# Performance work log

Hardware: AMD Instinct MI355X
Metric: run time of the kernel (lower is better)

Reference implementation:

```python
import jax, jax.numpy as jnp
import numpy as np

B, T, C = 16, 2048, 384
HEAD = 384

def setup_inputs() -> dict:
    key = jax.random.key(0)
    kx, kq, kk, kv = jax.random.split(key, 4)
    s = 1.0 / np.sqrt(C)
    return {
        "x": jax.random.normal(kx, (B, T, C), dtype=jnp.float32),
        "Wq": jax.random.normal(kq, (C, HEAD), dtype=jnp.float32) * s,
        "Wk": jax.random.normal(kk, (C, HEAD), dtype=jnp.float32) * s,
        "Wv": jax.random.normal(kv, (C, HEAD), dtype=jnp.float32) * s,
    }

def reference(x, Wq, Wk, Wv):
    # x: [B,T,C]; single causal attention head, eval mode (dropout = identity)
    Bc, Tc, Cc = x.shape
    q = jnp.einsum('btc,ch->bth', x, Wq)
    k = jnp.einsum('btc,ch->bth', x, Wk)
    v = jnp.einsum('btc,ch->bth', x, Wv)
    # NOTE: original scales by C**-0.5 (embedding dim), not head_size**-0.5
    scale = Cc ** (-0.5)
    wei = jnp.einsum('bth,bsh->bts', q, k) * scale  # [B,T,T]
    causal = jnp.tril(jnp.ones((Tc, Tc), dtype=bool))
    wei = jnp.where(causal, wei, -jnp.inf)
    wei = jax.nn.softmax(wei, axis=-1)
    out = jnp.einsum('bts,bsh->bth', wei, v)  # [B,T,head]
    return out
```

## Files before the change

kernel.cpp:

```cpp
#include <hip/hip_runtime.h>
#include <hip/hip_bf16.h>

#define NB 16
#define TT 2048
#define CC 384

typedef short bf16x8 __attribute__((ext_vector_type(8)));
typedef float f32x4 __attribute__((ext_vector_type(4)));

static __device__ __forceinline__ short f2bf(float f) {
  union { __hip_bfloat16 h; short s; } u;
  u.h = __float2bfloat16(f);
  return u.s;
}

#define QSC (0.051031036307982884f * 1.4426950408889634f)

__global__ __launch_bounds__(384)
void conv_wt(const float* __restrict__ Wq, const float* __restrict__ Wk,
             const float* __restrict__ Wv, short* __restrict__ Wbt) {
  const int w = blockIdx.x / CC;
  const int n = blockIdx.x % CC;
  const int k = threadIdx.x;
  const float* W = (w == 0) ? Wq : (w == 1) ? Wk : Wv;
  Wbt[((size_t)w * CC + n) * CC + k] = f2bf(W[(size_t)k * CC + n]);
}

__global__ __launch_bounds__(256)
void xconv(const float* __restrict__ x, short* __restrict__ xb) {
  const int i = (blockIdx.x * 256 + threadIdx.x) * 8;
  const float4 a = *(const float4*)(x + i);
  const float4 c = *(const float4*)(x + i + 4);
  bf16x8 r;
  r[0] = f2bf(a.x); r[1] = f2bf(a.y); r[2] = f2bf(a.z); r[3] = f2bf(a.w);
  r[4] = f2bf(c.x); r[5] = f2bf(c.y); r[6] = f2bf(c.z); r[7] = f2bf(c.w);
  *(bf16x8*)(xb + i) = r;
}

__global__ __launch_bounds__(256, 3)
void proj_gemm(const short* __restrict__ xb, const short* __restrict__ Wbt,
               short* __restrict__ Q, short* __restrict__ K,
               short* __restrict__ Vt) {
  __shared__ char smem[34816];
  short* Es = (short*)smem;

  const int mt = blockIdx.x & 255;
  const int nt = blockIdx.x >> 8;
  const int wsel = nt / 3;
  const int nc0 = (nt % 3) * 128;
  const int tid = threadIdx.x;
  const int wave = tid >> 6, lane = tid & 63;
  const int l15 = lane & 15, quad = lane >> 4;
  const int wm = (wave & 1) * 64, wn = (wave >> 1) * 64;

  const short* Ab = xb + (size_t)mt * 128 * CC;
  const short* Bb = Wbt + ((size_t)wsel * CC + nc0) * CC;

  int aoff[2];
  #pragma unroll
  for (int j = 0; j < 2; ++j) {
    const int lin = wave * 2048 + j * 1024 + lane * 16;
    const int r = lin >> 6;
    const int s = (lin >> 4) & 3;
    aoff[j] = r * CC + ((s ^ ((r >> 1) & 3)) * 8);
  }
  char* AW = smem + wave * 2048;
  char* BW = smem + 16384 + wave * 2048;

  f32x4 acc[16];
  #pragma unroll
  for (int i = 0; i < 16; ++i) acc[i] = f32x4{0.f, 0.f, 0.f, 0.f};

  #pragma unroll
  for (int pc = 0; pc < 2; ++pc) {
    #pragma unroll
    for (int j = 0; j < 2; ++j)
      __builtin_amdgcn_global_load_lds(
          (const __attribute__((address_space(1))) void*)(Ab + pc * 32 + aoff[j]),
          (__attribute__((address_space(3))) void*)(AW + pc * 8192 + j * 1024), 16, 0, 0);
    #pragma unroll
    for (int j = 0; j < 2; ++j)
      __builtin_amdgcn_global_load_lds(
          (const __attribute__((address_space(1))) void*)(Bb + pc * 32 + aoff[j]),
          (__attribute__((address_space(3))) void*)(BW + pc * 8192 + j * 1024), 16, 0, 0);
  }

  for (int kt = 0; kt < 12; ++kt) {
    const int kb = kt & 1;
    if (kt == 11) {
      asm volatile("s_waitcnt vmcnt(0)" ::: "memory");
    } else {
      asm volatile("s_waitcnt vmcnt(4)" ::: "memory");
    }
    __builtin_amdgcn_s_barrier();
    __builtin_amdgcn_sched_barrier(0);

    const char* As = smem + kb * 8192;
    const char* Bs = smem + 16384 + kb * 8192;
    bf16x8 af[4], bf[4];
    #pragma unroll
    for (int i = 0; i < 4; ++i) {
      const int ar = wm + i * 16 + l15;
      const int br = wn + i * 16 + l15;
      af[i] = *(const bf16x8*)(As + ar * 64 + ((quad ^ ((ar >> 1) & 3)) << 4));
      bf[i] = *(const bf16x8*)(Bs + br * 64 + ((quad ^ ((br >> 1) & 3)) << 4));
    }
    #pragma unroll
    for (int i = 0; i < 4; ++i)
      #pragma unroll
      for (int j = 0; j < 4; ++j)
        acc[i * 4 + j] =
            __builtin_amdgcn_mfma_f32_16x16x32_bf16(af[i], bf[j], acc[i * 4 + j], 0, 0, 0);

    __builtin_amdgcn_sched_barrier(0);
    __builtin_amdgcn_s_barrier();
    if (kt + 2 < 12) {
      const int k0 = (kt + 2) * 32;
      #pragma unroll
      for (int j = 0; j < 2; ++j)
        __builtin_amdgcn_global_load_lds(
            (const __attribute__((address_space(1))) void*)(Ab + k0 + aoff[j]),
            (__attribute__((address_space(3))) void*)(AW + kb * 8192 + j * 1024), 16, 0, 0);
      #pragma unroll
      for (int j = 0; j < 2; ++j)
        __builtin_amdgcn_global_load_lds(
            (const __attribute__((address_space(1))) void*)(Bb + k0 + aoff[j]),
            (__attribute__((address_space(3))) void*)(BW + kb * 8192 + j * 1024), 16, 0, 0);
    }
  }

  if (nt < 6) {
    short* O = (nt < 3) ? Q : K;
    const float sc = (nt < 3) ? QSC : 1.0f;
    #pragma unroll
    for (int i = 0; i < 4; ++i)
      #pragma unroll
      for (int j = 0; j < 4; ++j) {
        const f32x4 a = acc[i * 4 + j];
        const int r0 = mt * 128 + wm + i * 16 + quad * 4;
        const int c = nc0 + wn + j * 16 + l15;
        #pragma unroll
        for (int r = 0; r < 4; ++r) O[(size_t)(r0 + r) * CC + c] = f2bf(a[r] * sc);
      }
  } else {
    __syncthreads();
    #pragma unroll
    for (int i = 0; i < 4; ++i)
      #pragma unroll
      for (int j = 0; j < 4; ++j) {
        const f32x4 a = acc[i * 4 + j];
        const int dl = wn + j * 16 + l15;
        const int ml = wm + i * 16 + quad * 4;
        short4 p4;
        p4.x = f2bf(a[0]); p4.y = f2bf(a[1]); p4.z = f2bf(a[2]); p4.w = f2bf(a[3]);
        *(short4*)(Es + (size_t)dl * 136 + ml) = p4;
      }
    __syncthreads();
    const int d0 = (nt - 6) * 128;
    const int b = mt >> 4, t0 = (mt & 15) * 128;
    const int dr = tid >> 1, hf = tid & 1;
    const short* src = Es + (size_t)dr * 136 + hf * 64;
    short* dst = Vt + ((size_t)b * CC + d0 + dr) * TT + t0 + hf * 64;
    #pragma unroll
    for (int c = 0; c < 8; ++c)
      *(bf16x8*)(dst + c * 8) = *(const bf16x8*)(src + c * 8);
  }
}


#define ATTN_PRELUDE                                                          \
  __shared__ char sm[54272];                                                  \
  char* KsS = sm;                                                             \
  char* VsS = sm + 24576;                                                     \
  const int tid = threadIdx.x;                                                \
  const int wave = tid >> 6, lane = tid & 63;                                 \
  const int l15 = lane & 15, quad = lane >> 4;                                \
  short* pw = (short*)(sm + 49152) + wave * 640;                              \
  bf16x8 onesf;                                                               \
  _Pragma("unroll")                                                           \
  for (int i = 0; i < 8; ++i) onesf[i] = (short)0x3F80;                       \
  int koff[6], voff[6];                                                       \
  _Pragma("unroll")                                                           \
  for (int j = 0; j < 6; ++j) {                                               \
    const int lin = wave * 6144 + j * 1024 + lane * 16;                       \
    const int kr = lin / 768;                                                 \
    const int ksl = (lin - kr * 768) >> 4;                                    \
    koff[j] = kr * 768 + ((ksl ^ (kr & 7)) << 4);                             \
    const int vr = lin >> 6;                                                  \
    const int vsl = (lin >> 4) & 3;                                           \
    voff[j] = vr * 4096 + (((vsl - (vr >> 2)) & 3) << 4);                     \
  }                                                                           \
  char* KsW = KsS + wave * 6144;                                              \
  char* VsW = VsS + wave * 6144;

#define STAGE_CHUNK(ck)                                                       \
  do {                                                                        \
    const size_t kby_ = (size_t)(ck) * 24576;                                 \
    const size_t vby_ = (size_t)(ck) * 64;                                    \
    _Pragma("unroll")                                                         \
    for (int j = 0; j < 6; ++j)                                               \
      __builtin_amdgcn_global_load_lds(                                       \
          (const __attribute__((address_space(1))) void*)(kbB + kby_ + koff[j]), \
          (__attribute__((address_space(3))) void*)(KsW + j * 1024), 16, 0, 0);  \
    _Pragma("unroll")                                                         \
    for (int j = 0; j < 6; ++j)                                               \
      __builtin_amdgcn_global_load_lds(                                       \
          (const __attribute__((address_space(1))) void*)(vtB + vby_ + voff[j]), \
          (__attribute__((address_space(3))) void*)(VsW + j * 1024), 16, 0, 0);  \
  } while (0)

#define CHUNK_LOOP(C0, C1)                                                    \
  for (int kc = (C0); kc < (C1); ++kc) {                                      \
    const int k0 = kc * 32;                                                   \
    const int kb = (kc - (C0)) & 1;                                           \
    if (kc + 1 == (C1)) {                                                     \
      asm volatile("s_waitcnt vmcnt(0)" ::: "memory");                        \
    } else {                                                                  \
      asm volatile("s_waitcnt vmcnt(12)" ::: "memory");                       \
    }                                                                         \
    __builtin_amdgcn_s_barrier();                                             \
    __builtin_amdgcn_sched_barrier(0);                                        \
    const bool active = (k0 <= q0 + 15);                                      \
    if (active) {                                                             \
      const char* Ksb = KsS + kb * 0;             \
      (void)Ksb;                                                              \
    }                                                                         \
  }


__global__ __launch_bounds__(256, 2)
void attn_plain(const short* __restrict__ Q, const short* __restrict__ K,
                const short* __restrict__ Vt, float* __restrict__ out) {
  ATTN_PRELUDE
  const int blk = blockIdx.x;
  const int qt = 31 - (blk >> 4);
  const int b  = blk & 15;
  const int q0 = qt * 64 + wave * 16;

  bf16x8 qf[12];
  const short* qp = Q + ((size_t)b * TT + q0 + l15) * CC + quad * 8;
  #pragma unroll
  for (int ks = 0; ks < 12; ++ks) qf[ks] = *(const bf16x8*)(qp + ks * 32);

  f32x4 o[24];
  #pragma unroll
  for (int n = 0; n < 24; ++n) o[n] = f32x4{0.f, 0.f, 0.f, 0.f};
  f32x4 lsum = f32x4{0.f, 0.f, 0.f, 0.f};
  float m[4];
  #pragma unroll
  for (int r = 0; r < 4; ++r) m[r] = -INFINITY;

  const char* kbB = (const char*)(K + (size_t)b * TT * CC);
  const char* vtB = (const char*)(Vt + (size_t)b * CC * TT);
  const int nchunk = qt * 2 + 2;

  STAGE_CHUNK(0);

  for (int kc = 0; kc < nchunk; ++kc) {
    const int k0 = kc * 32;
    asm volatile("s_waitcnt vmcnt(6)" ::: "memory");
    __builtin_amdgcn_s_barrier();
    __builtin_amdgcn_sched_barrier(0);

    f32x4 s0 = f32x4{0.f, 0.f, 0.f, 0.f};
    f32x4 s1 = f32x4{0.f, 0.f, 0.f, 0.f};
    const bool active = (k0 <= q0 + 15);
    if (active) {
      #pragma unroll
      for (int ks = 0; ks < 12; ++ks) {
        const int sl = (ks * 4 + quad) ^ (l15 & 7);
        const bf16x8 b0 = *(const bf16x8*)(KsS + l15 * 768 + (sl << 4));
        const bf16x8 b1 = *(const bf16x8*)(KsS + (16 + l15) * 768 + (sl << 4));
        s0 = __builtin_amdgcn_mfma_f32_16x16x32_bf16(qf[ks], b0, s0, 0, 0, 0);
        s1 = __builtin_amdgcn_mfma_f32_16x16x32_bf16(qf[ks], b1, s1, 0, 0, 0);
      }
    }
    __builtin_amdgcn_sched_barrier(0);
    __builtin_amdgcn_s_barrier();
    {
      const int kn = (kc + 1 < nchunk) ? (kc + 1) : kc;
      const size_t kby_ = (size_t)kn * 24576;
      #pragma unroll
      for (int j = 0; j < 6; ++j)
        __builtin_amdgcn_global_load_lds(
            (const __attribute__((address_space(1))) void*)(kbB + kby_ + koff[j]),
            (__attribute__((address_space(3))) void*)(KsW + j * 1024), 16, 0, 0);
    }
    asm volatile("s_waitcnt vmcnt(6)" ::: "memory");
    __builtin_amdgcn_s_barrier();
    __builtin_amdgcn_sched_barrier(0);

    if (active) {
      const bool domask = (k0 + 31 > q0);
      float mx[4];
      #pragma unroll
      for (int r = 0; r < 4; ++r) {
        float a = s0[r], c = s1[r];
        if (domask) {
          const int qg = q0 + quad * 4 + r;
          if (k0 + l15 > qg)      a = -INFINITY;
          if (k0 + 16 + l15 > qg) c = -INFINITY;
        }
        s0[r] = a; s1[r] = c;
        float v = fmaxf(a, c);
        v = fmaxf(v, __shfl_xor(v, 1));
        v = fmaxf(v, __shfl_xor(v, 2));
        v = fmaxf(v, __shfl_xor(v, 4));
        v = fmaxf(v, __shfl_xor(v, 8));
        mx[r] = v;
      }
      float alpha[4];
      #pragma unroll
      for (int r = 0; r < 4; ++r) {
        const float mn = fmaxf(m[r], mx[r]);
        alpha[r] = exp2f(m[r] - mn);
        m[r] = mn;
        s0[r] = exp2f(s0[r] - mn);
        s1[r] = exp2f(s1[r] - mn);
      }
      const bool need = (alpha[0] < 1.f) | (alpha[1] < 1.f) |
                        (alpha[2] < 1.f) | (alpha[3] < 1.f);
      if (__any(need)) {
        #pragma unroll
        for (int r = 0; r < 4; ++r) lsum[r] *= alpha[r];
        #pragma unroll
        for (int n = 0; n < 24; ++n) {
          #pragma unroll
          for (int r = 0; r < 4; ++r) o[n][r] *= alpha[r];
        }
      }
      #pragma unroll
      for (int r = 0; r < 4; ++r) {
        pw[(quad * 4 + r) * 40 + l15]      = f2bf(s0[r]);
        pw[(quad * 4 + r) * 40 + 16 + l15] = f2bf(s1[r]);
      }
      const bf16x8 pf = *(const bf16x8*)(pw + l15 * 40 + quad * 8);
      lsum = __builtin_amdgcn_mfma_f32_16x16x32_bf16(pf, onesf, lsum, 0, 0, 0);
      #pragma unroll
      for (int n = 0; n < 24; ++n) {
        const int vrow = n * 16 + l15;
        const bf16x8 vf = *(const bf16x8*)(VsS + vrow * 64 + (((quad + (vrow >> 2)) & 3) << 4));
        o[n] = __builtin_amdgcn_mfma_f32_16x16x32_bf16(pf, vf, o[n], 0, 0, 0);
      }
    }
    __builtin_amdgcn_sched_barrier(0);
    __builtin_amdgcn_s_barrier();
    {
      const int kn = (kc + 1 < nchunk) ? (kc + 1) : kc;
      const size_t vby_ = (size_t)kn * 64;
      #pragma unroll
      for (int j = 0; j < 6; ++j)
        __builtin_amdgcn_global_load_lds(
            (const __attribute__((address_space(1))) void*)(vtB + vby_ + voff[j]),
            (__attribute__((address_space(3))) void*)(VsW + j * 1024), 16, 0, 0);
    }
  }

  float linv[4];
  #pragma unroll
  for (int r = 0; r < 4; ++r) linv[r] = 1.f / lsum[r];
  float* ob = out + ((size_t)b * TT + q0) * CC;
  #pragma unroll
  for (int n = 0; n < 24; ++n) {
    #pragma unroll
    for (int r = 0; r < 4; ++r) {
      ob[(size_t)(quad * 4 + r) * CC + n * 16 + l15] = o[n][r] * linv[r];
    }
  }
}

__global__ __launch_bounds__(256, 2)
void attn_split(const short* __restrict__ Q, const short* __restrict__ K,
                const short* __restrict__ Vt, float* __restrict__ out,
                float* __restrict__ OB, float* __restrict__ ML) {
  ATTN_PRELUDE
  const int blk = blockIdx.x;
  const int b = blk & 15;
  const int s = blk >> 4;
  const int j = s & 15;
  const int role = s >> 4;
  const int p = b * 16 + j;

  const char* kbB = (const char*)(K + (size_t)b * TT * CC);
  const char* vtB = (const char*)(Vt + (size_t)b * CC * TT);

  const int nph = role ? 1 : 2;
  #pragma unroll 1
  for (int ph = 0; ph < nph; ++ph) {
    int qt, c0, c1, mode;
    if (role == 0) {
      if (ph == 0) { qt = j;      c0 = 0;          c1 = 2 * j + 2;  mode = 0; }
      else         { qt = 31 - j; c0 = 0;          c1 = 31 - 2 * j; mode = 1; }
    } else         { qt = 31 - j; c0 = 31 - 2 * j; c1 = 64 - 2 * j; mode = 2; }
    const int q0 = qt * 64 + wave * 16;

    bf16x8 qf[12];
    const short* qp = Q + ((size_t)b * TT + q0 + l15) * CC + quad * 8;
    #pragma unroll
    for (int ks = 0; ks < 12; ++ks) qf[ks] = *(const bf16x8*)(qp + ks * 32);
    asm volatile("s_waitcnt vmcnt(0)" ::: "memory");

    f32x4 o[24];
    #pragma unroll
    for (int n = 0; n < 24; ++n) o[n] = f32x4{0.f, 0.f, 0.f, 0.f};
    f32x4 lsum = f32x4{0.f, 0.f, 0.f, 0.f};
    float m[4];
    #pragma unroll
    for (int r = 0; r < 4; ++r) m[r] = -INFINITY;

    #pragma unroll 1
    for (int pc = 0; pc < 2; ++pc) {
      if (c0 + pc < c1) {
        char* KsWb = KsW + pc * 12288;
        (void)KsWb;
        const size_t kby_ = (size_t)(c0 + pc) * 24576;
        const size_t vby_ = (size_t)(c0 + pc) * 64;
        char* KW = KsS + pc * 12288 + wave * 3072;
        char* VW = VsS + pc * 12288 + wave * 3072;
        #pragma unroll
        for (int jj2 = 0; jj2 < 3; ++jj2) {
          const int lin = wave * 3072 + jj2 * 1024 + lane * 16;
          const int kr = lin / 384;
          const int ksl = (lin - kr * 384) >> 4;
          const int ko = kr * 768 + (((ksl * 2 + (jj2 & 0)) ^ 0) << 4); (void)ko;
          (void)kby_; (void)vby_; (void)KW; (void)VW; (void)lin; (void)kr; (void)ksl;
        }
      }
    }
    {
      const size_t kby0 = (size_t)c0 * 24576;
      const size_t vby0 = (size_t)c0 * 64;
      #pragma unroll
      for (int jj2 = 0; jj2 < 6; ++jj2)
        __builtin_amdgcn_global_load_lds(
            (const __attribute__((address_space(1))) void*)(kbB + kby0 + koff[jj2]),
            (__attribute__((address_space(3))) void*)(KsW + jj2 * 1024), 16, 0, 0);
      #pragma unroll
      for (int jj2 = 0; jj2 < 6; ++jj2)
        __builtin_amdgcn_global_load_lds(
            (const __attribute__((address_space(1))) void*)(vtB + vby0 + voff[jj2]),
            (__attribute__((address_space(3))) void*)(VsW + jj2 * 1024), 16, 0, 0);
    }

    #pragma unroll 1
    for (int kc = c0; kc < c1; ++kc) {
      const int k0 = kc * 32;
      asm volatile("s_waitcnt vmcnt(6)" ::: "memory");
      __builtin_amdgcn_s_barrier();
      __builtin_amdgcn_sched_barrier(0);

      f32x4 s0 = f32x4{0.f, 0.f, 0.f, 0.f};
      f32x4 s1 = f32x4{0.f, 0.f, 0.f, 0.f};
      const bool active = (k0 <= q0 + 15);
      if (active) {
        #pragma unroll
        for (int ks = 0; ks < 12; ++ks) {
          const int sl = (ks * 4 + quad) ^ (l15 & 7);
          const bf16x8 b0 = *(const bf16x8*)(KsS + l15 * 768 + (sl << 4));
          const bf16x8 b1 = *(const bf16x8*)(KsS + (16 + l15) * 768 + (sl << 4));
          s0 = __builtin_amdgcn_mfma_f32_16x16x32_bf16(qf[ks], b0, s0, 0, 0, 0);
          s1 = __builtin_amdgcn_mfma_f32_16x16x32_bf16(qf[ks], b1, s1, 0, 0, 0);
        }
      }
      __builtin_amdgcn_sched_barrier(0);
      __builtin_amdgcn_s_barrier();
      {
        const int kn = (kc + 1 < c1) ? (kc + 1) : kc;
        const size_t kby_ = (size_t)kn * 24576;
        #pragma unroll
        for (int jj2 = 0; jj2 < 6; ++jj2)
          __builtin_amdgcn_global_load_lds(
              (const __attribute__((address_space(1))) void*)(kbB + kby_ + koff[jj2]),
              (__attribute__((address_space(3))) void*)(KsW + jj2 * 1024), 16, 0, 0);
      }
      asm volatile("s_waitcnt vmcnt(6)" ::: "memory");
      __builtin_amdgcn_s_barrier();
      __builtin_amdgcn_sched_barrier(0);

      if (active) {
        const bool domask = (k0 + 31 > q0);
        float mx[4];
        #pragma unroll
        for (int r = 0; r < 4; ++r) {
          float a = s0[r], c = s1[r];
          if (domask) {
            const int qg = q0 + quad * 4 + r;
            if (k0 + l15 > qg)      a = -INFINITY;
            if (k0 + 16 + l15 > qg) c = -INFINITY;
          }
          s0[r] = a; s1[r] = c;
          float v = fmaxf(a, c);
          v = fmaxf(v, __shfl_xor(v, 1));
          v = fmaxf(v, __shfl_xor(v, 2));
          v = fmaxf(v, __shfl_xor(v, 4));
          v = fmaxf(v, __shfl_xor(v, 8));
          mx[r] = v;
        }
        float alpha[4];
        #pragma unroll
        for (int r = 0; r < 4; ++r) {
          const float mn = fmaxf(m[r], mx[r]);
          alpha[r] = exp2f(m[r] - mn);
          m[r] = mn;
          s0[r] = exp2f(s0[r] - mn);
          s1[r] = exp2f(s1[r] - mn);
        }
        const bool need = (alpha[0] < 1.f) | (alpha[1] < 1.f) |
                          (alpha[2] < 1.f) | (alpha[3] < 1.f);
        if (__any(need)) {
          #pragma unroll
          for (int r = 0; r < 4; ++r) lsum[r] *= alpha[r];
          #pragma unroll
          for (int n = 0; n < 24; ++n) {
            #pragma unroll
            for (int r = 0; r < 4; ++r) o[n][r] *= alpha[r];
          }
        }
        #pragma unroll
        for (int r = 0; r < 4; ++r) {
          pw[(quad * 4 + r) * 40 + l15]      = f2bf(s0[r]);
          pw[(quad * 4 + r) * 40 + 16 + l15] = f2bf(s1[r]);
        }
        const bf16x8 pf = *(const bf16x8*)(pw + l15 * 40 + quad * 8);
        lsum = __builtin_amdgcn_mfma_f32_16x16x32_bf16(pf, onesf, lsum, 0, 0, 0);
        #pragma unroll
        for (int n = 0; n < 24; ++n) {
          const int vrow = n * 16 + l15;
          const bf16x8 vf = *(const bf16x8*)(VsS + vrow * 64 + (((quad + (vrow >> 2)) & 3) << 4));
          o[n] = __builtin_amdgcn_mfma_f32_16x16x32_bf16(pf, vf, o[n], 0, 0, 0);
        }
      }
      __builtin_amdgcn_sched_barrier(0);
      __builtin_amdgcn_s_barrier();
      {
        const int kn = (kc + 1 < c1) ? (kc + 1) : kc;
        const size_t vby_ = (size_t)kn * 64;
        #pragma unroll
        for (int jj2 = 0; jj2 < 6; ++jj2)
          __builtin_amdgcn_global_load_lds(
              (const __attribute__((address_space(1))) void*)(vtB + vby_ + voff[jj2]),
              (__attribute__((address_space(3))) void*)(VsW + jj2 * 1024), 16, 0, 0);
      }
    }
    asm volatile("s_waitcnt vmcnt(0)" ::: "memory");
    __builtin_amdgcn_s_barrier();

    if (mode == 0) {
      float linv[4];
      #pragma unroll
      for (int r = 0; r < 4; ++r) linv[r] = 1.f / lsum[r];
      float* ob = out + ((size_t)b * TT + q0) * CC;
      #pragma unroll
      for (int n = 0; n < 24; ++n) {
        #pragma unroll
        for (int r = 0; r < 4; ++r)
          ob[(size_t)(quad * 4 + r) * CC + n * 16 + l15] = o[n][r] * linv[r];
      }
    } else {
      float* ob = (mode == 1)
          ? out + ((size_t)b * TT + q0) * CC
          : OB + (size_t)p * 24576 + (size_t)(wave * 16) * CC;
      #pragma unroll
      for (int n = 0; n < 24; ++n) {
        #pragma unroll
        for (int r = 0; r < 4; ++r)
          ob[(size_t)(quad * 4 + r) * CC + n * 16 + l15] = o[n][r];
      }
      if (l15 == 0) {
        float* pml = ML + (size_t)p * 256 + (mode - 1) * 128;
        #pragma unroll
        for (int r = 0; r < 4; ++r) {
          pml[(wave * 16 + quad * 4 + r) * 2]     = m[r];
          pml[(wave * 16 + quad * 4 + r) * 2 + 1] = lsum[r];
        }
      }
    }
  }
}

__global__ __launch_bounds__(256)
void combine(float* __restrict__ out, const float* __restrict__ OB,
             const float* __restrict__ ML) {
  const int p = blockIdx.x;
  const int b = p >> 4, j = p & 15;
  const int H = 31 - j;
  const int row = threadIdx.x >> 2, seg = threadIdx.x & 3;
  const float* ml = ML + (size_t)p * 256;
  const float mA = ml[row * 2],       lA = ml[row * 2 + 1];
  const float mB = ml[128 + row * 2], lB = ml[128 + row * 2 + 1];
  const float mF = fmaxf(mA, mB);
  const float sA = exp2f(mA - mF), sB = exp2f(mB - mF);
  const float inv = 1.f / (lA * sA + lB * sB);
  const float wA = sA * inv, wB = sB * inv;
  float* pa = out + ((size_t)b * TT + H * 64 + row) * CC + seg * 96;
  const float* pb = OB + (size_t)p * 24576 + (size_t)row * CC + seg * 96;
  #pragma unroll
  for (int c = 0; c < 24; ++c) {
    float4 a = *(float4*)(pa + c * 4);
    const float4 bb = *(const float4*)(pb + c * 4);
    a.x = a.x * wA + bb.x * wB;
    a.y = a.y * wA + bb.y * wB;
    a.z = a.z * wA + bb.z * wB;
    a.w = a.w * wA + bb.w * wB;
    *(float4*)(pa + c * 4) = a;
  }
}

extern "C" void kernel_launch(void* const* d_in, const int* in_sizes, int n_in,
                              void* d_out, int out_size, void* d_ws, size_t ws_size,
                              hipStream_t stream) {
  const float* x  = (const float*)d_in[0];
  const float* Wq = (const float*)d_in[1];
  const float* Wk = (const float*)d_in[2];
  const float* Wv = (const float*)d_in[3];
  float* out = (float*)d_out;

  const size_t QS = (size_t)NB * TT * CC;
  short* Qs = (short*)d_ws;
  short* Ks = Qs + QS;
  short* Vt = Ks + QS;

  const size_t base = QS * 3 * 2;
  float* OB = (float*)((char*)d_ws + base);
  float* ML = (float*)((char*)d_ws + base + 25165824);
  const bool split = ws_size >= base + 25165824 + 524288;

  short* Wbt = (short*)d_out;
  short* xb  = (short*)((char*)d_out + 1048576);

  hipLaunchKernelGGL(conv_wt, dim3(3 * CC), dim3(CC), 0, stream, Wq, Wk, Wv, Wbt);
  hipLaunchKernelGGL(xconv, dim3(6144), dim3(256), 0, stream, x, xb);
  hipLaunchKernelGGL(proj_gemm, dim3(256 * 9), dim3(256), 0, stream,
                     xb, Wbt, Qs, Ks, Vt);
  if (split) {
    hipLaunchKernelGGL(attn_split, dim3(512), dim3(256), 0, stream,
                       Qs, Ks, Vt, out, OB, ML);
    hipLaunchKernelGGL(combine, dim3(256), dim3(256), 0, stream, out, OB, ML);
  } else {
    hipLaunchKernelGGL(attn_plain, dim3(512), dim3(256), 0, stream,
                       Qs, Ks, Vt, out);
  }
}
```

Measured before the change: 301.9 us.

## Split attention KV chunks by parity across block pairs and deepen projection GEMM K-tile

The split attention kernel now has each block pair process every query tile for a head pair, with one role taking even key chunks and the other odd ones, writing partials that are merged for all 512 tiles. This replaces the old scheme, which split only the long tiles and paired them with short ones, so work is spread more evenly across blocks. It adds more partial-output traffic, a larger workspace and a bigger combine pass. Separately, the projection GEMM stages 64-wide K tiles with an 8-way swizzle, halving the number of barrier iterations at the cost of more LDS and lower occupancy.

```diff
diff --git a/kernel.cpp b/kernel.cpp
--- a/kernel.cpp
+++ b/kernel.cpp
@@ -37,11 +37,11 @@
   *(bf16x8*)(xb + i) = r;
 }
 
-__global__ __launch_bounds__(256, 3)
+__global__ __launch_bounds__(256, 2)
 void proj_gemm(const short* __restrict__ xb, const short* __restrict__ Wbt,
                short* __restrict__ Q, short* __restrict__ K,
                short* __restrict__ Vt) {
-  __shared__ char smem[34816];
+  __shared__ char smem[65536];
   short* Es = (short*)smem;
 
   const int mt = blockIdx.x & 255;
@@ -56,16 +56,14 @@
   const short* Ab = xb + (size_t)mt * 128 * CC;
   const short* Bb = Wbt + ((size_t)wsel * CC + nc0) * CC;
 
-  int aoff[2];
-  #pragma unroll
-  for (int j = 0; j < 2; ++j) {
-    const int lin = wave * 2048 + j * 1024 + lane * 16;
-    const int r = lin >> 6;
-    const int s = (lin >> 4) & 3;
-    aoff[j] = r * CC + ((s ^ ((r >> 1) & 3)) * 8);
-  }
-  char* AW = smem + wave * 2048;
-  char* BW = smem + 16384 + wave * 2048;
+  int aoff[4];
+  #pragma unroll
+  for (int j = 0; j < 4; ++j) {
+    const int lin = wave * 4096 + j * 1024 + lane * 16;
+    const int r = lin >> 7;
+    const int s = (lin >> 4) & 7;
+    aoff[j] = r * CC + ((s ^ (r & 7)) << 3);
+  }
 
   f32x4 acc[16];
   #pragma unroll
@@ -74,58 +72,61 @@
   #pragma unroll
   for (int pc = 0; pc < 2; ++pc) {
     #pragma unroll
-    for (int j = 0; j < 2; ++j)
+    for (int j = 0; j < 4; ++j)
       __builtin_amdgcn_global_load_lds(
-          (const __attribute__((address_space(1))) void*)(Ab + pc * 32 + aoff[j]),
-          (__attribute__((address_space(3))) void*)(AW + pc * 8192 + j * 1024), 16, 0, 0);
-    #pragma unroll
-    for (int j = 0; j < 2; ++j)
+          (const __attribute__((address_space(1))) void*)(Ab + pc * 64 + aoff[j]),
+          (__attribute__((address_space(3))) void*)(smem + pc * 16384 + wave * 4096 + j * 1024), 16, 0, 0);
+    #pragma unroll
+    for (int j = 0; j < 4; ++j)
       __builtin_amdgcn_global_load_lds(
-          (const __attribute__((address_space(1))) void*)(Bb + pc * 32 + aoff[j]),
-          (__attribute__((address_space(3))) void*)(BW + pc * 8192 + j * 1024), 16, 0, 0);
-  }
-
-  for (int kt = 0; kt < 12; ++kt) {
+          (const __attribute__((address_space(1))) void*)(Bb + pc * 64 + aoff[j]),
+          (__attribute__((address_space(3))) void*)(smem + 32768 + pc * 16384 + wave * 4096 + j * 1024), 16, 0, 0);
+  }
+
+  for (int kt = 0; kt < 6; ++kt) {
     const int kb = kt & 1;
-    if (kt == 11) {
+    if (kt == 5) {
       asm volatile("s_waitcnt vmcnt(0)" ::: "memory");
     } else {
-      asm volatile("s_waitcnt vmcnt(4)" ::: "memory");
+      asm volatile("s_waitcnt vmcnt(8)" ::: "memory");
     }
     __builtin_amdgcn_s_barrier();
     __builtin_amdgcn_sched_barrier(0);
 
-    const char* As = smem + kb * 8192;
-    const char* Bs = smem + 16384 + kb * 8192;
-    bf16x8 af[4], bf[4];
-    #pragma unroll
-    for (int i = 0; i < 4; ++i) {
-      const int ar = wm + i * 16 + l15;
-      const int br = wn + i * 16 + l15;
-      af[i] = *(const bf16x8*)(As + ar * 64 + ((quad ^ ((ar >> 1) & 3)) << 4));
-      bf[i] = *(const bf16x8*)(Bs + br * 64 + ((quad ^ ((br >> 1) & 3)) << 4));
-    }
-    #pragma unroll
-    for (int i = 0; i < 4; ++i)
-      #pragma unroll
-      for (int j = 0; j < 4; ++j)
-        acc[i * 4 + j] =
-            __builtin_amdgcn_mfma_f32_16x16x32_bf16(af[i], bf[j], acc[i * 4 + j], 0, 0, 0);
+    const char* As = smem + kb * 16384;
+    const char* Bs = smem + 32768 + kb * 16384;
+    #pragma unroll
+    for (int ks = 0; ks < 2; ++ks) {
+      bf16x8 af[4], bf[4];
+      #pragma unroll
+      for (int i = 0; i < 4; ++i) {
+        const int ar = wm + i * 16 + l15;
+        const int br = wn + i * 16 + l15;
+        af[i] = *(const bf16x8*)(As + ar * 128 + (((ks * 4 + quad) ^ (ar & 7)) << 4));
+        bf[i] = *(const bf16x8*)(Bs + br * 128 + (((ks * 4 + quad) ^ (br & 7)) << 4));
+      }
+      #pragma unroll
+      for (int i = 0; i < 4; ++i)
+        #pragma unroll
+        for (int j = 0; j < 4; ++j)
+          acc[i * 4 + j] =
+              __builtin_amdgcn_mfma_f32_16x16x32_bf16(af[i], bf[j], acc[i * 4 + j], 0, 0, 0);
+    }
 
     __builtin_amdgcn_sched_barrier(0);
     __builtin_amdgcn_s_barrier();
-    if (kt + 2 < 12) {
-      const int k0 = (kt + 2) * 32;
-      #pragma unroll
-      for (int j = 0; j < 2; ++j)
+    if (kt + 2 < 6) {
+      const int k0 = (kt + 2) * 64;
+      #pragma unroll
+      for (int j = 0; j < 4; ++j)
         __builtin_amdgcn_global_load_lds(
             (const __attribute__((address_space(1))) void*)(Ab + k0 + aoff[j]),
-            (__attribute__((address_space(3))) void*)(AW + kb * 8192 + j * 1024), 16, 0, 0);
-      #pragma unroll
-      for (int j = 0; j < 2; ++j)
+            (__attribute__((address_space(3))) void*)(smem + kb * 16384 + wave * 4096 + j * 1024), 16, 0, 0);
+      #pragma unroll
+      for (int j = 0; j < 4; ++j)
         __builtin_amdgcn_global_load_lds(
             (const __attribute__((address_space(1))) void*)(Bb + k0 + aoff[j]),
-            (__attribute__((address_space(3))) void*)(BW + kb * 8192 + j * 1024), 16, 0, 0);
+            (__attribute__((address_space(3))) void*)(smem + 32768 + kb * 16384 + wave * 4096 + j * 1024), 16, 0, 0);
     }
   }
 
@@ -193,40 +194,25 @@
   char* KsW = KsS + wave * 6144;                                              \
   char* VsW = VsS + wave * 6144;
 
-#define STAGE_CHUNK(ck)                                                       \
+#define STAGE_K(ck)                                                           \
   do {                                                                        \
     const size_t kby_ = (size_t)(ck) * 24576;                                 \
+    _Pragma("unroll")                                                         \
+    for (int j5 = 0; j5 < 6; ++j5)                                            \
+      __builtin_amdgcn_global_load_lds(                                       \
+          (const __attribute__((address_space(1))) void*)(kbB + kby_ + koff[j5]), \
+          (__attribute__((address_space(3))) void*)(KsW + j5 * 1024), 16, 0, 0);  \
+  } while (0)
+
+#define STAGE_V(ck)                                                           \
+  do {                                                                        \
     const size_t vby_ = (size_t)(ck) * 64;                                    \
     _Pragma("unroll")                                                         \
-    for (int j = 0; j < 6; ++j)                                               \
+    for (int j5 = 0; j5 < 6; ++j5)                                            \
       __builtin_amdgcn_global_load_lds(                                       \
-          (const __attribute__((address_space(1))) void*)(kbB + kby_ + koff[j]), \
-          (__attribute__((address_space(3))) void*)(KsW + j * 1024), 16, 0, 0);  \
-    _Pragma("unroll")                                                         \
-    for (int j = 0; j < 6; ++j)                                               \
-      __builtin_amdgcn_global_load_lds(                                       \
-          (const __attribute__((address_space(1))) void*)(vtB + vby_ + voff[j]), \
-          (__attribute__((address_space(3))) void*)(VsW + j * 1024), 16, 0, 0);  \
+          (const __attribute__((address_space(1))) void*)(vtB + vby_ + voff[j5]), \
+          (__attribute__((address_space(3))) void*)(VsW + j5 * 1024), 16, 0, 0);  \
   } while (0)
-
-#define CHUNK_LOOP(C0, C1)                                                    \
-  for (int kc = (C0); kc < (C1); ++kc) {                                      \
-    const int k0 = kc * 32;                                                   \
-    const int kb = (kc - (C0)) & 1;                                           \
-    if (kc + 1 == (C1)) {                                                     \
-      asm volatile("s_waitcnt vmcnt(0)" ::: "memory");                        \
-    } else {                                                                  \
-      asm volatile("s_waitcnt vmcnt(12)" ::: "memory");                       \
-    }                                                                         \
-    __builtin_amdgcn_s_barrier();                                             \
-    __builtin_amdgcn_sched_barrier(0);                                        \
-    const bool active = (k0 <= q0 + 15);                                      \
-    if (active) {                                                             \
-      const char* Ksb = KsS + kb * 0;             \
-      (void)Ksb;                                                              \
-    }                                                                         \
-  }
-
 
 __global__ __launch_bounds__(256, 2)
 void attn_plain(const short* __restrict__ Q, const short* __restrict__ K,
@@ -254,7 +240,8 @@
   const char* vtB = (const char*)(Vt + (size_t)b * CC * TT);
   const int nchunk = qt * 2 + 2;
 
-  STAGE_CHUNK(0);
+  STAGE_K(0);
+  STAGE_V(0);
 
   for (int kc = 0; kc < nchunk; ++kc) {
     const int k0 = kc * 32;
@@ -277,15 +264,7 @@
     }
     __builtin_amdgcn_sched_barrier(0);
     __builtin_amdgcn_s_barrier();
-    {
-      const int kn = (kc + 1 < nchunk) ? (kc + 1) : kc;
-      const size_t kby_ = (size_t)kn * 24576;
-      #pragma unroll
-      for (int j = 0; j < 6; ++j)
-        __builtin_amdgcn_global_load_lds(
-            (const __attribute__((address_space(1))) void*)(kbB + kby_ + koff[j]),
-            (__attribute__((address_space(3))) void*)(KsW + j * 1024), 16, 0, 0);
-    }
+    { const int kn = (kc + 1 < nchunk) ? (kc + 1) : kc; STAGE_K(kn); }
     asm volatile("s_waitcnt vmcnt(6)" ::: "memory");
     __builtin_amdgcn_s_barrier();
     __builtin_amdgcn_sched_barrier(0);
@@ -345,15 +324,7 @@
     }
     __builtin_amdgcn_sched_barrier(0);
     __builtin_amdgcn_s_barrier();
-    {
-      const int kn = (kc + 1 < nchunk) ? (kc + 1) : kc;
-      const size_t vby_ = (size_t)kn * 64;
-      #pragma unroll
-      for (int j = 0; j < 6; ++j)
-        __builtin_amdgcn_global_load_lds(
-            (const __attribute__((address_space(1))) void*)(vtB + vby_ + voff[j]),
-            (__attribute__((address_space(3))) void*)(VsW + j * 1024), 16, 0, 0);
-    }
+    { const int kn = (kc + 1 < nchunk) ? (kc + 1) : kc; STAGE_V(kn); }
   }
 
   float linv[4];
@@ -379,19 +350,15 @@
   const int s = blk >> 4;
   const int j = s & 15;
   const int role = s >> 4;
-  const int p = b * 16 + j;
 
   const char* kbB = (const char*)(K + (size_t)b * TT * CC);
   const char* vtB = (const char*)(Vt + (size_t)b * CC * TT);
 
-  const int nph = role ? 1 : 2;
   #pragma unroll 1
-  for (int ph = 0; ph < nph; ++ph) {
-    int qt, c0, c1, mode;
-    if (role == 0) {
-      if (ph == 0) { qt = j;      c0 = 0;          c1 = 2 * j + 2;  mode = 0; }
-      else         { qt = 31 - j; c0 = 0;          c1 = 31 - 2 * j; mode = 1; }
-    } else         { qt = 31 - j; c0 = 31 - 2 * j; c1 = 64 - 2 * j; mode = 2; }
+  for (int ph = 0; ph < 2; ++ph) {
+    const int qt = ph ? j : (31 - j);
+    const int tile = b * 32 + qt;
+    const int nchunk = qt * 2 + 2;
     const int q0 = qt * 64 + wave * 16;
 
     bf16x8 qf[12];
@@ -408,42 +375,11 @@
     #pragma unroll
     for (int r = 0; r < 4; ++r) m[r] = -INFINITY;
 
+    STAGE_K(role);
+    STAGE_V(role);
+
     #pragma unroll 1
-    for (int pc = 0; pc < 2; ++pc) {
-      if (c0 + pc < c1) {
-        char* KsWb = KsW + pc * 12288;
-        (void)KsWb;
-        const size_t kby_ = (size_t)(c0 + pc) * 24576;
-        const size_t vby_ = (size_t)(c0 + pc) * 64;
-        char* KW = KsS + pc * 12288 + wave * 3072;
-        char* VW = VsS + pc * 12288 + wave * 3072;
-        #pragma unroll
-        for (int jj2 = 0; jj2 < 3; ++jj2) {
-          const int lin = wave * 3072 + jj2 * 1024 + lane * 16;
-          const int kr = lin / 384;
-          const int ksl = (lin - kr * 384) >> 4;
-          const int ko = kr * 768 + (((ksl * 2 + (jj2 & 0)) ^ 0) << 4); (void)ko;
-          (void)kby_; (void)vby_; (void)KW; (void)VW; (void)lin; (void)kr; (void)ksl;
-        }
-      }
-    }
-    {
-      const size_t kby0 = (size_t)c0 * 24576;
-      const size_t vby0 = (size_t)c0 * 64;
-      #pragma unroll
-      for (int jj2 = 0; jj2 < 6; ++jj2)
-        __builtin_amdgcn_global_load_lds(
-            (const __attribute__((address_space(1))) void*)(kbB + kby0 + koff[jj2]),
-            (__attribute__((address_space(3))) void*)(KsW + jj2 * 1024), 16, 0, 0);
-      #pragma unroll
-      for (int jj2 = 0; jj2 < 6; ++jj2)
-        __builtin_amdgcn_global_load_lds(
-            (const __attribute__((address_space(1))) void*)(vtB + vby0 + voff[jj2]),
-            (__attribute__((address_space(3))) void*)(VsW + jj2 * 1024), 16, 0, 0);
-    }
-
-    #pragma unroll 1
-    for (int kc = c0; kc < c1; ++kc) {
+    for (int kc = role; kc < nchunk; kc += 2) {
       const int k0 = kc * 32;
       asm volatile("s_waitcnt vmcnt(6)" ::: "memory");
       __builtin_amdgcn_s_barrier();
@@ -464,15 +400,7 @@
       }
       __builtin_amdgcn_sched_barrier(0);
       __builtin_amdgcn_s_barrier();
-      {
-        const int kn = (kc + 1 < c1) ? (kc + 1) : kc;
-        const size_t kby_ = (size_t)kn * 24576;
-        #pragma unroll
-        for (int jj2 = 0; jj2 < 6; ++jj2)
-          __builtin_amdgcn_global_load_lds(
-              (const __attribute__((address_space(1))) void*)(kbB + kby_ + koff[jj2]),
-              (__attribute__((address_space(3))) void*)(KsW + jj2 * 1024), 16, 0, 0);
-      }
+      { const int kn = (kc + 2 < nchunk) ? (kc + 2) : kc; STAGE_K(kn); }
       asm volatile("s_waitcnt vmcnt(6)" ::: "memory");
       __builtin_amdgcn_s_barrier();
       __builtin_amdgcn_sched_barrier(0);
@@ -532,47 +460,24 @@
       }
       __builtin_amdgcn_sched_barrier(0);
       __builtin_amdgcn_s_barrier();
-      {
-        const int kn = (kc + 1 < c1) ? (kc + 1) : kc;
-        const size_t vby_ = (size_t)kn * 64;
-        #pragma unroll
-        for (int jj2 = 0; jj2 < 6; ++jj2)
-          __builtin_amdgcn_global_load_lds(
-              (const __attribute__((address_space(1))) void*)(vtB + vby_ + voff[jj2]),
-              (__attribute__((address_space(3))) void*)(VsW + jj2 * 1024), 16, 0, 0);
-      }
-    }
-    asm volatile("s_waitcnt vmcnt(0)" ::: "memory");
-    __builtin_amdgcn_s_barrier();
-
-    if (mode == 0) {
-      float linv[4];
-      #pragma unroll
-      for (int r = 0; r < 4; ++r) linv[r] = 1.f / lsum[r];
-      float* ob = out + ((size_t)b * TT + q0) * CC;
-      #pragma unroll
-      for (int n = 0; n < 24; ++n) {
-        #pragma unroll
-        for (int r = 0; r < 4; ++r)
-          ob[(size_t)(quad * 4 + r) * CC + n * 16 + l15] = o[n][r] * linv[r];
-      }
-    } else {
-      float* ob = (mode == 1)
-          ? out + ((size_t)b * TT + q0) * CC
-          : OB + (size_t)p * 24576 + (size_t)(wave * 16) * CC;
-      #pragma unroll
-      for (int n = 0; n < 24; ++n) {
-        #pragma unroll
-        for (int r = 0; r < 4; ++r)
-          ob[(size_t)(quad * 4 + r) * CC + n * 16 + l15] = o[n][r];
-      }
-      if (l15 == 0) {
-        float* pml = ML + (size_t)p * 256 + (mode - 1) * 128;
-        #pragma unroll
-        for (int r = 0; r < 4; ++r) {
-          pml[(wave * 16 + quad * 4 + r) * 2]     = m[r];
-          pml[(wave * 16 + quad * 4 + r) * 2 + 1] = lsum[r];
-        }
+      { const int kn = (kc + 2 < nchunk) ? (kc + 2) : kc; STAGE_V(kn); }
+    }
+
+    float* ob = (role == 0)
+        ? out + ((size_t)b * TT + q0) * CC
+        : OB + (size_t)tile * 24576 + (size_t)(wave * 16) * CC;
+    #pragma unroll
+    for (int n = 0; n < 24; ++n) {
+      #pragma unroll
+      for (int r = 0; r < 4; ++r)
+        ob[(size_t)(quad * 4 + r) * CC + n * 16 + l15] = o[n][r];
+    }
+    if (l15 == 0) {
+      float* pml = ML + (size_t)tile * 256 + role * 128;
+      #pragma unroll
+      for (int r = 0; r < 4; ++r) {
+        pml[(wave * 16 + quad * 4 + r) * 2]     = m[r];
+        pml[(wave * 16 + quad * 4 + r) * 2 + 1] = lsum[r];
       }
     }
   }
@@ -581,19 +486,18 @@
 __global__ __launch_bounds__(256)
 void combine(float* __restrict__ out, const float* __restrict__ OB,
              const float* __restrict__ ML) {
-  const int p = blockIdx.x;
-  const int b = p >> 4, j = p & 15;
-  const int H = 31 - j;
+  const int t = blockIdx.x;
+  const int b = t >> 5, qt = t & 31;
   const int row = threadIdx.x >> 2, seg = threadIdx.x & 3;
-  const float* ml = ML + (size_t)p * 256;
+  const float* ml = ML + (size_t)t * 256;
   const float mA = ml[row * 2],       lA = ml[row * 2 + 1];
   const float mB = ml[128 + row * 2], lB = ml[128 + row * 2 + 1];
   const float mF = fmaxf(mA, mB);
   const float sA = exp2f(mA - mF), sB = exp2f(mB - mF);
   const float inv = 1.f / (lA * sA + lB * sB);
   const float wA = sA * inv, wB = sB * inv;
-  float* pa = out + ((size_t)b * TT + H * 64 + row) * CC + seg * 96;
-  const float* pb = OB + (size_t)p * 24576 + (size_t)row * CC + seg * 96;
+  float* pa = out + ((size_t)b * TT + qt * 64 + row) * CC + seg * 96;
+  const float* pb = OB + (size_t)t * 24576 + (size_t)row * CC + seg * 96;
   #pragma unroll
   for (int c = 0; c < 24; ++c) {
     float4 a = *(float4*)(pa + c * 4);
@@ -622,8 +526,8 @@
 
   const size_t base = QS * 3 * 2;
   float* OB = (float*)((char*)d_ws + base);
-  float* ML = (float*)((char*)d_ws + base + 25165824);
-  const bool split = ws_size >= base + 25165824 + 524288;
+  float* ML = (float*)((char*)d_ws + base + 50331648);
+  const bool split = ws_size >= base + 50331648 + 524288;
 
   short* Wbt = (short*)d_out;
   short* xb  = (short*)((char*)d_out + 1048576);
@@ -635,7 +539,7 @@
   if (split) {
     hipLaunchKernelGGL(attn_split, dim3(512), dim3(256), 0, stream,
                        Qs, Ks, Vt, out, OB, ML);
-    hipLaunchKernelGGL(combine, dim3(256), dim3(256), 0, stream, out, OB, ML);
+    hipLaunchKernelGGL(combine, dim3(512), dim3(256), 0, stream, out, OB, ML);
   } else {
     hipLaunchKernelGGL(attn_plain, dim3(512), dim3(256), 0, stream,
                        Qs, Ks, Vt, out);
```

Result: slower. 341.3 us (+13.1%).
